# Performance work log

Hardware: AMD Instinct MI355X
Metric: run time of the kernel (lower is better)

## Reference

```python
import jax, jax.numpy as jnp
import numpy as np

N_NODES = 50000
HEADS = 8
NEG_SLOPE = 0.2


def _gat_conv(x, src, dst, n, W, a_src, a_dst, b, concat):
    # W: [H*C, F_in], a_src/a_dst: [H, C], b: [H*C] or [C]
    H, C = a_src.shape
    h = (x @ W.T).reshape(-1, H, C)                      # [N, H, C]
    al_src = jnp.einsum('nhc,hc->nh', h, a_src)          # [N, H]
    al_dst = jnp.einsum('nhc,hc->nh', h, a_dst)          # [N, H]
    e = jax.nn.leaky_relu(al_src[src] + al_dst[dst], NEG_SLOPE)  # [E, H]
    # segment softmax over incoming edges of each dst node
    m = jax.lax.stop_gradient(jax.ops.segment_max(e, dst, num_segments=n))
    ee = jnp.exp(e - m[dst])
    denom = jax.ops.segment_sum(ee, dst, num_segments=n)
    alpha = ee / denom[dst]                              # [E, H]
    out = jax.ops.segment_sum(alpha[:, :, None] * h[src], dst, num_segments=n)  # [N, H, C]
    out = out.reshape(n, H * C) if concat else out.mean(axis=1)
    return out + b


def setup_inputs() -> dict:
    key = jax.random.key(0)
    ks = jax.random.split(key, 12)
    N, F_in, Hd, H, Ncls = N_NODES, 128, 32, HEADS, 40
    E = 800000
    x = jax.random.normal(ks[0], (N, F_in), dtype=jnp.float32)
    edge_index = jax.random.randint(ks[1], (2, E), 0, N, dtype=jnp.int64)
    s1 = 1.0 / np.sqrt(F_in)
    W1 = jax.random.normal(ks[2], (H * Hd, F_in), dtype=jnp.float32) * s1
    a_src1 = jax.random.normal(ks[3], (H, Hd), dtype=jnp.float32) * 0.1
    a_dst1 = jax.random.normal(ks[4], (H, Hd), dtype=jnp.float32) * 0.1
    b1 = jnp.zeros((H * Hd,), dtype=jnp.float32)
    s2 = 1.0 / np.sqrt(H * Hd)
    W2 = jax.random.normal(ks[5], (H * Ncls, H * Hd), dtype=jnp.float32) * s2
    a_src2 = jax.random.normal(ks[6], (H, Ncls), dtype=jnp.float32) * 0.1
    a_dst2 = jax.random.normal(ks[7], (H, Ncls), dtype=jnp.float32) * 0.1
    b2 = jnp.zeros((Ncls,), dtype=jnp.float32)
    return {"x": x, "edge_index": edge_index,
            "W1": W1, "a_src1": a_src1, "a_dst1": a_dst1, "b1": b1,
            "W2": W2, "a_src2": a_src2, "a_dst2": a_dst2, "b2": b2}


def reference(x, edge_index, W1, a_src1, a_dst1, b1, W2, a_src2, a_dst2, b2):
    n = x.shape[0]
    # PyG GATConv default: add self loops
    loop = jnp.arange(n, dtype=edge_index.dtype)
    src = jnp.concatenate([edge_index[0], loop])
    dst = jnp.concatenate([edge_index[1], loop])
    # layer 1 (concat heads) -> ELU; dropout identity in eval mode
    h = _gat_conv(x, src, dst, n, W1, a_src1, a_dst1, b1, concat=True)
    h = jax.nn.elu(h)
    # layer 2 (mean over heads)
    out = _gat_conv(h, src, dst, n, W2, a_src2, a_dst2, b2, concat=False)
    return jax.nn.log_softmax(out, axis=1)
```

## Files before the change

kernel.cpp:

```cpp
#include <hip/hip_runtime.h>
#include <hip/hip_bf16.h>
#include <math.h>

typedef unsigned short ushort_t;
typedef unsigned char uchar_t;
typedef __attribute__((ext_vector_type(8))) short short8;
typedef __attribute__((ext_vector_type(4))) float f32x4;
typedef __attribute__((ext_vector_type(2))) float f32x2;
typedef __attribute__((ext_vector_type(4))) unsigned short u16x4;

#define LOG2E 1.44269504088896f

static __device__ __forceinline__ float b2f(ushort_t u) {
    union { unsigned int i; float f; } v; v.i = ((unsigned int)u) << 16; return v.f;
}
static __device__ __forceinline__ ushort_t f2b(float f) {
    unsigned int x = __float_as_uint(f);
    unsigned int r = (x + 0x7fffu + ((x >> 16) & 1u)) >> 16;
    return (ushort_t)r;
}
static __device__ __forceinline__ uchar_t f2e4m3(float f) {
    int r = __builtin_amdgcn_cvt_pk_fp8_f32(f, f, 0, false);
    return (uchar_t)(r & 0xff);
}
static __device__ __forceinline__ float exp2fast(float x) {
    return __builtin_amdgcn_exp2f(x);
}


template<int K, int Cd>
static __device__ void wa_item(const float* __restrict__ W, const float* __restrict__ as,
                               const float* __restrict__ ad, ushort_t* __restrict__ Bext,
                               int rowoff, int tid) {
    int col = tid / K, k = tid - col * K;
    const float* a = (col < 8) ? as : ad;
    int h = col & 7;
    float s = 0.f;
    #pragma unroll 4
    for (int c = 0; c < Cd; ++c)
        s += W[(size_t)(h * Cd + c) * K + k] * a[h * Cd + c];
    Bext[(size_t)(rowoff + col) * K + k] = f2b(s * LOG2E);
}

__global__ void prep_kernel(const float* __restrict__ W1, const float* __restrict__ W2,
                            const float* __restrict__ as1, const float* __restrict__ ad1,
                            const float* __restrict__ as2, const float* __restrict__ ad2,
                            ushort_t* __restrict__ w1b, ushort_t* __restrict__ w2b,
                            float* als1, float* als2, uchar_t* h1f8, uchar_t* h2f8, int n) {
    int b = blockIdx.x, t = threadIdx.x;
    if (b < 40) {
        for (int i = b * 256 + t; i < 8192 + 20480; i += 40 * 256) {
            if (i < 8192) {
                float4 v = *(const float4*)(W1 + i * 4);
                u16x4 o = { f2b(v.x), f2b(v.y), f2b(v.z), f2b(v.w) };
                *(u16x4*)(w1b + i * 4) = o;
            } else {
                int j = i - 8192;
                float4 v = *(const float4*)(W2 + j * 4);
                u16x4 o = { f2b(v.x), f2b(v.y), f2b(v.z), f2b(v.w) };
                *(u16x4*)(w2b + j * 4) = o;
            }
        }
    } else if (b < 64) {
        for (int i = (b - 40) * 256 + t; i < 2048 + 4096; i += 24 * 256) {
            if (i < 2048) wa_item<128, 32>(W1, as1, ad1, w1b, 256, i);
            else          wa_item<256, 40>(W2, as2, ad2, w2b, 320, i - 2048);
        }
    } else {
        if (t < 8) { als1[(size_t)n * 8 + t] = -1e30f; als2[(size_t)n * 8 + t] = -1e30f; }
        h1f8[(size_t)n * 256 + t] = 0;
        h2f8[(size_t)n * 320 + t] = 0;
        if (t < 64) h2f8[(size_t)n * 320 + 256 + t] = 0;
    }
}


__global__ void convx_count_kernel(const float* __restrict__ x, ushort_t* __restrict__ xb, int n4x,
                                   const int* __restrict__ ei, int E, int n, int* __restrict__ deg) {
    int b = blockIdx.x, t = threadIdx.x;
    if (b < 2048) {
        for (int i = b * 256 + t; i < n4x; i += 2048 * 256) {
            float4 v = *(const float4*)(x + i * 4);
            u16x4 o = { f2b(v.x), f2b(v.y), f2b(v.z), f2b(v.w) };
            *(u16x4*)(xb + i * 4) = o;
        }
    } else {
        int e = (b - 2048) * 256 + t;
        int Etot = E + n;
        if (e < Etot) {
            int dst = (e < E) ? ei[E + e] : (e - E);
            atomicAdd(&deg[dst], 1);
        }
    }
}


__global__ void scan_kernel(const int* __restrict__ deg, int* __restrict__ rowptr,
                            int* __restrict__ cursor, int n) {
    __shared__ int wsum[16];
    int t = threadIdx.x;
    int lane = t & 63, wid = t >> 6;
    int carry = 0;
    for (int base = 0; base < n; base += 1024) {
        int i = base + t;
        int v = (i < n) ? ((deg[i] + 7) & ~7) : 0;
        int val = v;
        #pragma unroll
        for (int off = 1; off < 64; off <<= 1) {
            int nv = __shfl_up(val, off);
            if (lane >= off) val += nv;
        }
        if (lane == 63) wsum[wid] = val;
        __syncthreads();
        int wpre = 0, tot = 0;
        #pragma unroll
        for (int w = 0; w < 16; ++w) {
            int s = wsum[w];
            if (w < wid) wpre += s;
            tot += s;
        }
        int excl = carry + wpre + val - v;
        if (i < n) { rowptr[i] = excl; cursor[i] = excl; }
        carry += tot;
        __syncthreads();
    }
    if (t == 0) rowptr[n] = carry;
}

__global__ void scatter_kernel(const int* __restrict__ ei, int E, int n,
                               int* __restrict__ cursor, int* __restrict__ ssrc) {
    int e = blockIdx.x * blockDim.x + threadIdx.x;
    int Etot = E + n;
    if (e >= Etot) return;
    int src, dst;
    if (e < E) { src = ei[e]; dst = ei[E + e]; }
    else       { src = e - E; dst = e - E; }
    int pos = atomicAdd(&cursor[dst], 1);
    ssrc[pos] = src;
}

__global__ void pad_fill_kernel(const int* __restrict__ rowptr, const int* __restrict__ cursor,
                                int* __restrict__ ssrc, int n) {
    int i = blockIdx.x * blockDim.x + threadIdx.x;
    if (i >= n) return;
    int p = cursor[i], e = rowptr[i + 1];
    for (; p < e; ++p) ssrc[p] = n;
}


template<int NFRAG, int K>
__global__ __launch_bounds__(512) void gemm_lds_al(const ushort_t* __restrict__ A,
                                                   const ushort_t* __restrict__ B,
                                                   uchar_t* __restrict__ C,
                                                   float* __restrict__ als,
                                                   float* __restrict__ ald, int M) {
    constexpr int N = NFRAG * 16;
    constexpr int NOUT = (NFRAG - 1) * 16;
    constexpr int RS = 40;
    constexpr int NK = K / 32;
    __shared__ ushort_t Bs[2][N * RS];
    const int t = threadIdx.x;
    const int w = t >> 6, l = t & 63;
    const int r0 = blockIdx.x * 128 + w * 16;
    int arow = r0 + (l & 15);
    if (arow >= M) arow = M - 1;
    const int koff = (l >> 4) * 8;
    const ushort_t* ap = A + (size_t)arow * K + koff;

    f32x4 acc[NFRAG];
    #pragma unroll
    for (int i = 0; i < NFRAG; ++i) acc[i] = (f32x4){0.f, 0.f, 0.f, 0.f};

    auto stage = [&](int buf, int k0) {
        #pragma unroll
        for (int c = t; c < N * 4; c += 512) {
            int row = c >> 2, part = (c & 3) << 3;
            *(short8*)&Bs[buf][row * RS + part] =
                *(const short8*)(B + (size_t)row * K + k0 + part);
        }
    };

    stage(0, 0);
    __syncthreads();
    #pragma unroll
    for (int kk = 0; kk < NK; ++kk) {
        int buf = kk & 1;
        if (kk + 1 < NK) stage(buf ^ 1, (kk + 1) * 32);
        short8 a = *(const short8*)(ap + kk * 32);
        #pragma unroll
        for (int nf = 0; nf < NFRAG; ++nf) {
            short8 b = *(const short8*)&Bs[buf][(nf * 16 + (l & 15)) * RS + koff];
            acc[nf] = __builtin_amdgcn_mfma_f32_16x16x32_bf16(a, b, acc[nf], 0, 0, 0);
        }
        __syncthreads();
    }

    const int crow0 = r0 + (l >> 4) * 4;
    #pragma unroll
    for (int nf = 0; nf < NFRAG - 1; ++nf) {
        #pragma unroll
        for (int j = 0; j < 4; ++j) {
            int row = crow0 + j;
            if (row < M) C[(size_t)row * NOUT + nf * 16 + (l & 15)] = f2e4m3(acc[nf][j]);
        }
    }
    {
        int col = l & 15;
        float* dstp = (col < 8) ? als : ald;
        int h = col & 7;
        #pragma unroll
        for (int j = 0; j < 4; ++j) {
            int row = crow0 + j;
            if (row < M) dstp[(size_t)row * 8 + h] = acc[NFRAG - 1][j];
        }
    }
}


__device__ __forceinline__ float lrelu(float e) { return (e > 0.f) ? e : 0.2f * e; }

__global__ void agg1_kernel(const uchar_t* __restrict__ h1, const float* __restrict__ als,
                            const float* __restrict__ aldv, const float* __restrict__ b1,
                            const int* __restrict__ rowptr, const int* __restrict__ ssrc,
                            ushort_t* __restrict__ hout, int n) {
    int node = blockIdx.x * 4 + (threadIdx.x >> 6);
    if (node >= n) return;
    int l = threadIdx.x & 63;
    int h = l >> 3;
    float ald = aldv[node * 8 + h];
    int beg = rowptr[node], end = rowptr[node + 1];
    float den = 0.f, a0 = 0.f, a1 = 0.f, a2 = 0.f, a3 = 0.f;
    for (int p = beg; p < end; p += 8) {
        int4 sA = *(const int4*)(ssrc + p);
        int4 sB = *(const int4*)(ssrc + p + 4);
        float w0 = exp2fast(lrelu(als[sA.x * 8 + h] + ald));
        float w1 = exp2fast(lrelu(als[sA.y * 8 + h] + ald));
        float w2 = exp2fast(lrelu(als[sA.z * 8 + h] + ald));
        float w3 = exp2fast(lrelu(als[sA.w * 8 + h] + ald));
        float w4 = exp2fast(lrelu(als[sB.x * 8 + h] + ald));
        float w5 = exp2fast(lrelu(als[sB.y * 8 + h] + ald));
        float w6 = exp2fast(lrelu(als[sB.z * 8 + h] + ald));
        float w7 = exp2fast(lrelu(als[sB.w * 8 + h] + ald));
        int g0 = *(const int*)(h1 + (size_t)sA.x * 256 + l * 4);
        int g1 = *(const int*)(h1 + (size_t)sA.y * 256 + l * 4);
        int g2 = *(const int*)(h1 + (size_t)sA.z * 256 + l * 4);
        int g3 = *(const int*)(h1 + (size_t)sA.w * 256 + l * 4);
        int g4 = *(const int*)(h1 + (size_t)sB.x * 256 + l * 4);
        int g5 = *(const int*)(h1 + (size_t)sB.y * 256 + l * 4);
        int g6 = *(const int*)(h1 + (size_t)sB.z * 256 + l * 4);
        int g7 = *(const int*)(h1 + (size_t)sB.w * 256 + l * 4);
        den += ((w0 + w1) + (w2 + w3)) + ((w4 + w5) + (w6 + w7));
        #define DQ(g, wv) { \
            f32x2 lo = __builtin_amdgcn_cvt_pk_f32_fp8(g, false); \
            f32x2 hi = __builtin_amdgcn_cvt_pk_f32_fp8(g, true);  \
            a0 += wv * lo.x; a1 += wv * lo.y; a2 += wv * hi.x; a3 += wv * hi.y; }
        DQ(g0, w0) DQ(g1, w1) DQ(g2, w2) DQ(g3, w3)
        DQ(g4, w4) DQ(g5, w5) DQ(g6, w6) DQ(g7, w7)
        #undef DQ
    }
    float inv = 1.f / den;
    float4 bv = *(const float4*)(b1 + l * 4);
    float v0 = a0 * inv + bv.x, v1 = a1 * inv + bv.y;
    float v2 = a2 * inv + bv.z, v3 = a3 * inv + bv.w;
    u16x4 o;
    o.x = f2b((v0 > 0.f) ? v0 : __expf(v0) - 1.f);
    o.y = f2b((v1 > 0.f) ? v1 : __expf(v1) - 1.f);
    o.z = f2b((v2 > 0.f) ? v2 : __expf(v2) - 1.f);
    o.w = f2b((v3 > 0.f) ? v3 : __expf(v3) - 1.f);
    *(u16x4*)(hout + (size_t)node * 256 + l * 4) = o;
}


__global__ void agg2_kernel(const uchar_t* __restrict__ h2, const float* __restrict__ als,
                            const float* __restrict__ aldv, const float* __restrict__ b2,
                            const int* __restrict__ rowptr, const int* __restrict__ ssrc,
                            float* __restrict__ out, int n) {
    int node = blockIdx.x * 4 + (threadIdx.x >> 6);
    if (node >= n) return;
    int l = threadIdx.x & 63;
    int li = (l < 40) ? l : 0;
    int hd = li / 5;
    int cg = li - hd * 5;
    float ald = aldv[node * 8 + hd];
    int beg = rowptr[node], end = rowptr[node + 1];
    const uchar_t* base = h2 + hd * 40 + cg * 8;
    float den = 0.f;
    float a0 = 0.f, a1 = 0.f, a2 = 0.f, a3 = 0.f, a4 = 0.f, a5 = 0.f, a6 = 0.f, a7 = 0.f;
    for (int p = beg; p < end; p += 8) {
        int4 sA = *(const int4*)(ssrc + p);
        int4 sB = *(const int4*)(ssrc + p + 4);
        float w0 = exp2fast(lrelu(als[sA.x * 8 + hd] + ald));
        float w1 = exp2fast(lrelu(als[sA.y * 8 + hd] + ald));
        float w2 = exp2fast(lrelu(als[sA.z * 8 + hd] + ald));
        float w3 = exp2fast(lrelu(als[sA.w * 8 + hd] + ald));
        float w4 = exp2fast(lrelu(als[sB.x * 8 + hd] + ald));
        float w5 = exp2fast(lrelu(als[sB.y * 8 + hd] + ald));
        float w6 = exp2fast(lrelu(als[sB.z * 8 + hd] + ald));
        float w7 = exp2fast(lrelu(als[sB.w * 8 + hd] + ald));
        uint2 g0 = *(const uint2*)(base + (size_t)sA.x * 320);
        uint2 g1 = *(const uint2*)(base + (size_t)sA.y * 320);
        uint2 g2 = *(const uint2*)(base + (size_t)sA.z * 320);
        uint2 g3 = *(const uint2*)(base + (size_t)sA.w * 320);
        uint2 g4 = *(const uint2*)(base + (size_t)sB.x * 320);
        uint2 g5 = *(const uint2*)(base + (size_t)sB.y * 320);
        uint2 g6 = *(const uint2*)(base + (size_t)sB.z * 320);
        uint2 g7 = *(const uint2*)(base + (size_t)sB.w * 320);
        den += ((w0 + w1) + (w2 + w3)) + ((w4 + w5) + (w6 + w7));
        #define DQ(g, wv) { \
            f32x2 q0 = __builtin_amdgcn_cvt_pk_f32_fp8((int)g.x, false); \
            f32x2 q1 = __builtin_amdgcn_cvt_pk_f32_fp8((int)g.x, true);  \
            f32x2 q2 = __builtin_amdgcn_cvt_pk_f32_fp8((int)g.y, false); \
            f32x2 q3 = __builtin_amdgcn_cvt_pk_f32_fp8((int)g.y, true);  \
            a0 += wv * q0.x; a1 += wv * q0.y; a2 += wv * q1.x; a3 += wv * q1.y; \
            a4 += wv * q2.x; a5 += wv * q2.y; a6 += wv * q3.x; a7 += wv * q3.y; }
        DQ(g0, w0) DQ(g1, w1) DQ(g2, w2) DQ(g3, w3)
        DQ(g4, w4) DQ(g5, w5) DQ(g6, w6) DQ(g7, w7)
        #undef DQ
    }
    float inv = 1.f / den;
    float v[8] = {a0 * inv, a1 * inv, a2 * inv, a3 * inv,
                  a4 * inv, a5 * inv, a6 * inv, a7 * inv};
    #pragma unroll
    for (int j = 0; j < 8; ++j) {
        float s = v[j];
        s += __shfl_down(s, 20);
        s += __shfl_down(s, 10);
        s += __shfl_down(s, 5);
        v[j] = s;
    }
    if (l < 5) {
        float wv[8];
        #pragma unroll
        for (int j = 0; j < 8; ++j) wv[j] = 0.125f * v[j] + b2[l * 8 + j];
        float m8 = wv[0];
        #pragma unroll
        for (int j = 1; j < 8; ++j) m8 = fmaxf(m8, wv[j]);
        float mx = m8;
        #pragma unroll
        for (int k = 0; k < 5; ++k) mx = fmaxf(mx, __shfl(m8, k));
        float se8 = 0.f;
        #pragma unroll
        for (int j = 0; j < 8; ++j) se8 += __expf(wv[j] - mx);
        float se = 0.f;
        #pragma unroll
        for (int k = 0; k < 5; ++k) se += __shfl(se8, k);
        float lse = mx + __logf(se);
        float* op = out + (size_t)node * 40 + l * 8;
        float4 o0 = {wv[0] - lse, wv[1] - lse, wv[2] - lse, wv[3] - lse};
        float4 o1 = {wv[4] - lse, wv[5] - lse, wv[6] - lse, wv[7] - lse};
        *(float4*)op = o0;
        *(float4*)(op + 4) = o1;
    }
}


extern "C" void kernel_launch(void* const* d_in, const int* in_sizes, int n_in,
                              void* d_out, int out_size, void* d_ws, size_t ws_size,
                              hipStream_t stream) {
    const float* x      = (const float*)d_in[0];
    const int*   ei     = (const int*)d_in[1];
    const float* W1     = (const float*)d_in[2];
    const float* a_src1 = (const float*)d_in[3];
    const float* a_dst1 = (const float*)d_in[4];
    const float* b1     = (const float*)d_in[5];
    const float* W2     = (const float*)d_in[6];
    const float* a_src2 = (const float*)d_in[7];
    const float* a_dst2 = (const float*)d_in[8];
    const float* b2     = (const float*)d_in[9];
    float* out = (float*)d_out;

    const int n    = in_sizes[0] / 128;
    const int E    = in_sizes[1] / 2;
    const int Etot = E + n;
    const int EpM  = Etot + 7 * n + 16;

    char* w = (char*)d_ws;
    auto take = [&](size_t bytes) {
        char* p = w;
        w += (bytes + 255) & ~(size_t)255;
        return p;
    };
    int*      deg    = (int*)take((size_t)n * 4);
    int*      rowptr = (int*)take((size_t)(n + 1) * 4);
    int*      cursor = (int*)take((size_t)n * 4);
    int*      ssrc   = (int*)take((size_t)EpM * 4);
    ushort_t* xb     = (ushort_t*)take((size_t)n * 128 * 2);
    ushort_t* w1b    = (ushort_t*)take((size_t)272 * 128 * 2);
    ushort_t* w2b    = (ushort_t*)take((size_t)336 * 256 * 2);
    uchar_t*  h1f8   = (uchar_t*)take((size_t)(n + 1) * 256);
    ushort_t* helu   = (ushort_t*)take((size_t)n * 256 * 2);
    uchar_t*  h2f8   = (uchar_t*)take((size_t)(n + 1) * 320);
    float*    als1   = (float*)take((size_t)(n + 1) * 8 * 4);
    float*    ald1   = (float*)take((size_t)n * 8 * 4);
    float*    als2   = (float*)take((size_t)(n + 1) * 8 * 4);
    float*    ald2   = (float*)take((size_t)n * 8 * 4);

    hipMemsetAsync(deg, 0, (size_t)n * 4, stream);

    prep_kernel<<<65, 256, 0, stream>>>(W1, W2, a_src1, a_dst1, a_src2, a_dst2,
                                        w1b, w2b, als1, als2, h1f8, h2f8, n);

    int eb = (Etot + 255) / 256;
    convx_count_kernel<<<2048 + eb, 256, 0, stream>>>(x, xb, n * 128 / 4, ei, E, n, deg);
    scan_kernel<<<1, 1024, 0, stream>>>(deg, rowptr, cursor, n);
    scatter_kernel<<<eb, 256, 0, stream>>>(ei, E, n, cursor, ssrc);
    pad_fill_kernel<<<(n + 255) / 256, 256, 0, stream>>>(rowptr, cursor, ssrc, n);

    int gb = (n + 127) / 128;
    int nb4 = (n + 3) / 4;

    gemm_lds_al<17, 128><<<gb, 512, 0, stream>>>(xb, w1b, h1f8, als1, ald1, n);
    agg1_kernel<<<nb4, 256, 0, stream>>>(h1f8, als1, ald1, b1, rowptr, ssrc, helu, n);

    gemm_lds_al<21, 256><<<gb, 512, 0, stream>>>(helu, w2b, h2f8, als2, ald2, n);
    agg2_kernel<<<nb4, 256, 0, stream>>>(h2f8, als2, ald2, b2, rowptr, ssrc, out, n);
}
```

Measured before the change: 296.4 us.

## Parallelize degree scan across blocks and pack aggregation FMAs into f32x2

Replaces the single-block serial scan over 50k degrees with a three-pass multi-block scan: per-block sums, a top-level scan, and a write pass. This removes a long single-workgroup loop from the critical path at the cost of two extra kernel launches. Separately, the agg1 and agg2 accumulators become f32x2 vectors so the compiler can emit packed FMA instructions for the weighted fp8 gathers. The top-level scan handles at most 256 blocks, which limits n to 65536 nodes.

```diff
diff --git a/kernel.cpp b/kernel.cpp
--- a/kernel.cpp
+++ b/kernel.cpp
@@ -95,36 +95,56 @@
 }
 
 
-__global__ void scan_kernel(const int* __restrict__ deg, int* __restrict__ rowptr,
-                            int* __restrict__ cursor, int n) {
-    __shared__ int wsum[16];
+__global__ void scan_part_kernel(const int* __restrict__ deg, int* __restrict__ bsum, int n) {
+    int i = blockIdx.x * 256 + threadIdx.x;
+    int v = (i < n) ? ((deg[i] + 7) & ~7) : 0;
+    #pragma unroll
+    for (int off = 1; off < 64; off <<= 1) v += __shfl_xor(v, off);
+    __shared__ int ws[4];
+    int wid = threadIdx.x >> 6, lane = threadIdx.x & 63;
+    if (lane == 0) ws[wid] = v;
+    __syncthreads();
+    if (threadIdx.x == 0) bsum[blockIdx.x] = ws[0] + ws[1] + ws[2] + ws[3];
+}
+
+__global__ void scan_top_kernel(int* __restrict__ bsum, int nb) {
     int t = threadIdx.x;
+    int v = (t < nb) ? bsum[t] : 0;
+    int val = v;
     int lane = t & 63, wid = t >> 6;
-    int carry = 0;
-    for (int base = 0; base < n; base += 1024) {
-        int i = base + t;
-        int v = (i < n) ? ((deg[i] + 7) & ~7) : 0;
-        int val = v;
-        #pragma unroll
-        for (int off = 1; off < 64; off <<= 1) {
-            int nv = __shfl_up(val, off);
-            if (lane >= off) val += nv;
-        }
-        if (lane == 63) wsum[wid] = val;
-        __syncthreads();
-        int wpre = 0, tot = 0;
-        #pragma unroll
-        for (int w = 0; w < 16; ++w) {
-            int s = wsum[w];
-            if (w < wid) wpre += s;
-            tot += s;
-        }
-        int excl = carry + wpre + val - v;
-        if (i < n) { rowptr[i] = excl; cursor[i] = excl; }
-        carry += tot;
-        __syncthreads();
-    }
-    if (t == 0) rowptr[n] = carry;
+    #pragma unroll
+    for (int off = 1; off < 64; off <<= 1) {
+        int nv = __shfl_up(val, off);
+        if (lane >= off) val += nv;
+    }
+    __shared__ int ws[4];
+    if (lane == 63) ws[wid] = val;
+    __syncthreads();
+    int pre = 0;
+    for (int w = 0; w < 4; ++w) if (w < wid) pre += ws[w];
+    if (t < nb) bsum[t] = pre + val - v;
+}
+
+__global__ void scan_write_kernel(const int* __restrict__ deg, const int* __restrict__ bsum,
+                                  int* __restrict__ rowptr, int* __restrict__ cursor, int n) {
+    int i = blockIdx.x * 256 + threadIdx.x;
+    int t = threadIdx.x;
+    int v = (i < n) ? ((deg[i] + 7) & ~7) : 0;
+    int val = v;
+    int lane = t & 63, wid = t >> 6;
+    #pragma unroll
+    for (int off = 1; off < 64; off <<= 1) {
+        int nv = __shfl_up(val, off);
+        if (lane >= off) val += nv;
+    }
+    __shared__ int ws[4];
+    if (lane == 63) ws[wid] = val;
+    __syncthreads();
+    int pre = bsum[blockIdx.x];
+    for (int w = 0; w < 4; ++w) if (w < wid) pre += ws[w];
+    int excl = pre + val - v;
+    if (i < n) { rowptr[i] = excl; cursor[i] = excl; }
+    if (i == n - 1) rowptr[n] = excl + v;
 }
 
 __global__ void scatter_kernel(const int* __restrict__ ei, int E, int n,
@@ -229,7 +249,8 @@
     int h = l >> 3;
     float ald = aldv[node * 8 + h];
     int beg = rowptr[node], end = rowptr[node + 1];
-    float den = 0.f, a0 = 0.f, a1 = 0.f, a2 = 0.f, a3 = 0.f;
+    float den = 0.f;
+    f32x2 acc01 = {0.f, 0.f}, acc23 = {0.f, 0.f};
     for (int p = beg; p < end; p += 8) {
         int4 sA = *(const int4*)(ssrc + p);
         int4 sB = *(const int4*)(ssrc + p + 4);
@@ -253,15 +274,16 @@
         #define DQ(g, wv) { \
             f32x2 lo = __builtin_amdgcn_cvt_pk_f32_fp8(g, false); \
             f32x2 hi = __builtin_amdgcn_cvt_pk_f32_fp8(g, true);  \
-            a0 += wv * lo.x; a1 += wv * lo.y; a2 += wv * hi.x; a3 += wv * hi.y; }
+            f32x2 w2v = {wv, wv}; \
+            acc01 += w2v * lo; acc23 += w2v * hi; }
         DQ(g0, w0) DQ(g1, w1) DQ(g2, w2) DQ(g3, w3)
         DQ(g4, w4) DQ(g5, w5) DQ(g6, w6) DQ(g7, w7)
         #undef DQ
     }
     float inv = 1.f / den;
     float4 bv = *(const float4*)(b1 + l * 4);
-    float v0 = a0 * inv + bv.x, v1 = a1 * inv + bv.y;
-    float v2 = a2 * inv + bv.z, v3 = a3 * inv + bv.w;
+    float v0 = acc01.x * inv + bv.x, v1 = acc01.y * inv + bv.y;
+    float v2 = acc23.x * inv + bv.z, v3 = acc23.y * inv + bv.w;
     u16x4 o;
     o.x = f2b((v0 > 0.f) ? v0 : __expf(v0) - 1.f);
     o.y = f2b((v1 > 0.f) ? v1 : __expf(v1) - 1.f);
@@ -285,7 +307,7 @@
     int beg = rowptr[node], end = rowptr[node + 1];
     const uchar_t* base = h2 + hd * 40 + cg * 8;
     float den = 0.f;
-    float a0 = 0.f, a1 = 0.f, a2 = 0.f, a3 = 0.f, a4 = 0.f, a5 = 0.f, a6 = 0.f, a7 = 0.f;
+    f32x2 acc01 = {0.f, 0.f}, acc23 = {0.f, 0.f}, acc45 = {0.f, 0.f}, acc67 = {0.f, 0.f};
     for (int p = beg; p < end; p += 8) {
         int4 sA = *(const int4*)(ssrc + p);
         int4 sB = *(const int4*)(ssrc + p + 4);
@@ -311,15 +333,16 @@
             f32x2 q1 = __builtin_amdgcn_cvt_pk_f32_fp8((int)g.x, true);  \
             f32x2 q2 = __builtin_amdgcn_cvt_pk_f32_fp8((int)g.y, false); \
             f32x2 q3 = __builtin_amdgcn_cvt_pk_f32_fp8((int)g.y, true);  \
-            a0 += wv * q0.x; a1 += wv * q0.y; a2 += wv * q1.x; a3 += wv * q1.y; \
-            a4 += wv * q2.x; a5 += wv * q2.y; a6 += wv * q3.x; a7 += wv * q3.y; }
+            f32x2 w2v = {wv, wv}; \
+            acc01 += w2v * q0; acc23 += w2v * q1; \
+            acc45 += w2v * q2; acc67 += w2v * q3; }
         DQ(g0, w0) DQ(g1, w1) DQ(g2, w2) DQ(g3, w3)
         DQ(g4, w4) DQ(g5, w5) DQ(g6, w6) DQ(g7, w7)
         #undef DQ
     }
     float inv = 1.f / den;
-    float v[8] = {a0 * inv, a1 * inv, a2 * inv, a3 * inv,
-                  a4 * inv, a5 * inv, a6 * inv, a7 * inv};
+    float v[8] = {acc01.x * inv, acc01.y * inv, acc23.x * inv, acc23.y * inv,
+                  acc45.x * inv, acc45.y * inv, acc67.x * inv, acc67.y * inv};
     #pragma unroll
     for (int j = 0; j < 8; ++j) {
         float s = v[j];
@@ -373,6 +396,7 @@
     const int E    = in_sizes[1] / 2;
     const int Etot = E + n;
     const int EpM  = Etot + 7 * n + 16;
+    const int nb   = (n + 255) / 256;
 
     char* w = (char*)d_ws;
     auto take = [&](size_t bytes) {
@@ -383,6 +407,7 @@
     int*      deg    = (int*)take((size_t)n * 4);
     int*      rowptr = (int*)take((size_t)(n + 1) * 4);
     int*      cursor = (int*)take((size_t)n * 4);
+    int*      bsum   = (int*)take((size_t)(nb + 1) * 4);
     int*      ssrc   = (int*)take((size_t)EpM * 4);
     ushort_t* xb     = (ushort_t*)take((size_t)n * 128 * 2);
     ushort_t* w1b    = (ushort_t*)take((size_t)272 * 128 * 2);
@@ -402,7 +427,9 @@
 
     int eb = (Etot + 255) / 256;
     convx_count_kernel<<<2048 + eb, 256, 0, stream>>>(x, xb, n * 128 / 4, ei, E, n, deg);
-    scan_kernel<<<1, 1024, 0, stream>>>(deg, rowptr, cursor, n);
+    scan_part_kernel<<<nb, 256, 0, stream>>>(deg, bsum, n);
+    scan_top_kernel<<<1, 256, 0, stream>>>(bsum, nb);
+    scan_write_kernel<<<nb, 256, 0, stream>>>(deg, bsum, rowptr, cursor, n);
     scatter_kernel<<<eb, 256, 0, stream>>>(ei, E, n, cursor, ssrc);
     pad_fill_kernel<<<(n + 255) / 256, 256, 0, stream>>>(rowptr, cursor, ssrc, n);
 
```

Measured after the change: 258.2 us. 1.15x faster.
